# Kernel tuning notes

Measured on AMD Instinct MI355X. Metric: run time of the kernel, lower is better.

Reference implementation:

```python
import jax, jax.numpy as jnp
import numpy as np

B, NPER, H = 32, 512, 32
N, E = B * NPER, 65536
IN_CH, EDGE_CH, L1, L2, NL = 100, 16, 64, 64, 4


def setup_inputs() -> dict:
    key = jax.random.key(0)
    ks = jax.random.split(key, 14)
    f = lambda k, s: jax.random.normal(k, s, dtype=jnp.float32) * 0.1
    return {
        "x_nodes": jax.random.randint(ks[0], (N,), 0, IN_CH),
        "edge_index": jax.random.randint(ks[1], (2, E), 0, N),
        "edge_attr": jax.random.randint(ks[2], (E,), 0, EDGE_CH),
        "metal_idx": jax.random.randint(ks[3], (B,), 0, NPER),
        "loop_edge": jax.random.randint(ks[4], (B, L1, 2), 0, NPER),
        "loop_pair": jax.random.randint(ks[5], (B, L2, 2), 0, NPER),
        "node_emb": f(ks[6], (IN_CH, H)),
        "edge_emb": f(ks[7], (NL, EDGE_CH, 8)),
        "lin_w": f(ks[8], (NL, 8, H * H)),
        "lin_b": f(ks[9], (NL, H * H)),
        "root_w": f(ks[10], (NL, H, H)),
        "conv_b": f(ks[11], (NL, H)),
        "f_w": f(ks[12], (H, 1)),
        "f_b": f(ks[13], (1,)),
    }


def reference(x_nodes, edge_index, edge_attr, metal_idx, loop_edge, loop_pair,
              node_emb, edge_emb, lin_w, lin_b, root_w, conv_b, f_w, f_b):
    src, dst = edge_index[0], edge_index[1]
    # mean-aggregation denominator (clamped to 1 for isolated nodes, as PyG)
    deg = jax.ops.segment_sum(jnp.ones((E,), jnp.float32), dst, num_segments=N)
    denom = jnp.maximum(deg, 1.0)[:, None]

    x = node_emb[x_nodes]  # [N,H]
    for l in range(NL):
        # edge nn: Embedding -> ReLU -> Linear(8, H*H)
        e8 = jax.nn.relu(edge_emb[l][edge_attr])              # [E,8]
        W = (e8 @ lin_w[l] + lin_b[l]).reshape(E, H, H)       # [E,H,H]
        msg = jnp.einsum('ei,eio->eo', x[src], W)             # [E,H]
        agg = jax.ops.segment_sum(msg, dst, num_segments=N) / denom
        x_new = agg + x @ root_w[l] + conv_b[l]               # root weight + bias
        x = jax.nn.relu(x_new) if l < NL - 1 else x_new

    metal_g = metal_idx + jnp.arange(B) * NPER                # global metal node ids
    xm = x[metal_g]                                           # [B,H]
    fhM = (xm @ f_w + f_b)[:, 0]                              # [B]

    xg = x.reshape(B, NPER, H)
    bidx = jnp.arange(B)[:, None]

    def pair_prod(pairs):
        xs = xg[bidx, pairs[:, :, 0]]                         # [B,L,H]
        xt = xg[bidx, pairs[:, :, 1]]                         # [B,L,H]
        # sum(xm*xs) + sum(xm*xt) + sum(xs*(-xt))
        return jnp.sum(xm[:, None, :] * (xs + xt) - xs * xt, axis=-1)

    res_edge = pair_prod(loop_edge) - fhM[:, None]            # [B,L1]
    res_pair = -pair_prod(loop_pair)                          # [B,L2]
    return jnp.concatenate([res_edge, res_pair], axis=1)      # [B, L1+L2]
```

## Files before the change

kernel.cpp:

```cpp
#include <hip/hip_runtime.h>

#define NN 16384
#define NE 65536
#define H  32
#define BB 32
#define NPERB 512

__global__ __launch_bounds__(256) void k_prep1(
    const int* __restrict__ x_nodes, const int* __restrict__ edge_index,
    const int* __restrict__ edge_attr, const float* __restrict__ node_emb,
    const float* __restrict__ edge_emb, const float* __restrict__ lin_w,
    const float* __restrict__ lin_b, float* __restrict__ x0, float* __restrict__ Wt,
    float* __restrict__ degf, int* __restrict__ tcount, float* __restrict__ zb1) {
    __shared__ int lh[16];
    int b = blockIdx.x, thr = threadIdx.x;
    if (b < 512) {
        int t = b * 256 + thr;
        int n = t >> 3, r = t & 7;
        int xn = x_nodes[n];
        ((float4*)x0)[t] = ((const float4*)node_emb)[xn * 8 + r];
    } else if (b < 768) {
        int w = (b - 512) * 256 + thr;
        int l = w >> 14, rest = w & 16383;
        int ty = rest >> 10, io = rest & 1023;
        float acc = lin_b[l * 1024 + io];
#pragma unroll
        for (int jj = 0; jj < 8; ++jj) {
            float e2 = fmaxf(edge_emb[(l * 16 + ty) * 8 + jj], 0.f);
            acc = fmaf(e2, lin_w[(l * 8 + jj) * 1024 + io], acc);
        }
        Wt[w] = acc;
    } else if (b < 1024) {
        if (thr < 16) lh[thr] = 0;
        __syncthreads();
        int e = (b - 768) * 256 + thr;
        int d = edge_index[NE + e];
        int ty = edge_attr[e];
        atomicAdd(&degf[d], 1.0f);
        atomicAdd(&lh[ty], 1);
        __syncthreads();
        if (thr < 16) atomicAdd(&tcount[thr], lh[thr]);
    } else {
        int z = (b - 1024) * 256 + thr;
        ((float4*)zb1)[z] = make_float4(0.f, 0.f, 0.f, 0.f);
    }
}

__global__ void k_prep2(const int* __restrict__ tcount, int* __restrict__ gcursor) {
    int t = threadIdx.x;
    int c = (t < 16) ? tcount[t] : 0;
    int base = 0;
    for (int u = 0; u < 15; ++u) {
        int cu = __shfl(c, u);
        if (u < t) base += cu;
    }
    if (t < 16) gcursor[t] = base;
}

__global__ __launch_bounds__(256) void k_prep3(
    const int* __restrict__ edge_index, const int* __restrict__ edge_attr,
    int* __restrict__ gcursor, unsigned int* __restrict__ blist) {
    __shared__ int lh[16], lb[16];
    int thr = threadIdx.x;
    if (thr < 16) lh[thr] = 0;
    __syncthreads();
    int e = blockIdx.x * 256 + thr;
    unsigned int s = (unsigned int)edge_index[e];
    unsigned int d = (unsigned int)edge_index[NE + e];
    int ty = edge_attr[e];
    int rank = atomicAdd(&lh[ty], 1);
    __syncthreads();
    if (thr < 16) lb[thr] = atomicAdd(&gcursor[thr], lh[thr]);
    __syncthreads();
    blist[lb[ty] + rank] = s | (d << 14) | ((unsigned int)ty << 28);
}

__global__ __launch_bounds__(256) void k_phase(
    const float* __restrict__ xin, float* __restrict__ xout, float* __restrict__ zb,
    const unsigned int* __restrict__ blist, const float* __restrict__ degf,
    const float* __restrict__ Wl, const float* __restrict__ Rl,
    const float* __restrict__ Bl, int relu_in) {
    int t = blockIdx.x * 256 + threadIdx.x;
    int base = threadIdx.x & 32;
    if (t < 2097152) {
        int e = t >> 5, o = t & 31;
        unsigned int p = blist[e];
        int s = p & 16383, d = (p >> 14) & 16383, ty = (int)(p >> 28);
        float xv = xin[s * H + o];
        if (relu_in) xv = fmaxf(xv, 0.f);
        float invd = __builtin_amdgcn_rcpf(fmaxf(degf[d], 1.0f));
        const float* __restrict__ W = Wl + ty * 1024 + o;
        float acc = 0.f;
#pragma unroll
        for (int i = 0; i < 32; ++i)
            acc = fmaf(__shfl(xv, base + i), W[i * 32], acc);
        atomicAdd(&xout[d * H + o], acc * invd);
    } else if (t < 2621440) {
        int t2 = t - 2097152;
        int o = t2 & 31;
        float xv = xin[t2];
        if (relu_in) xv = fmaxf(xv, 0.f);
        float acc = Bl[o];
#pragma unroll
        for (int i = 0; i < 32; ++i)
            acc = fmaf(__shfl(xv, base + i), Rl[i * 32 + o], acc);
        atomicAdd(&xout[t2], acc);
    } else if (zb) {
        zb[t - 2621440] = 0.f;
    }
}

__global__ void k_final(const float* __restrict__ x, const int* __restrict__ metal_idx,
                        const int* __restrict__ loop_edge, const int* __restrict__ loop_pair,
                        const float* __restrict__ f_w, const float* __restrict__ f_b,
                        float* __restrict__ out) {
    int tid = blockIdx.x * blockDim.x + threadIdx.x;
    if (tid >= BB * 128) return;
    int b = tid >> 7, j = tid & 127;
    int mg = metal_idx[b] + b * NPERB;
    const float* __restrict__ xm = x + mg * H;
    int p0, p1;
    if (j < 64) {
        p0 = loop_edge[(b * 64 + j) * 2];
        p1 = loop_edge[(b * 64 + j) * 2 + 1];
    } else {
        int j2 = j - 64;
        p0 = loop_pair[(b * 64 + j2) * 2];
        p1 = loop_pair[(b * 64 + j2) * 2 + 1];
    }
    const float* __restrict__ xs = x + (b * NPERB + p0) * H;
    const float* __restrict__ xt = x + (b * NPERB + p1) * H;
    float fh = f_b[0];
    float pp = 0.f;
#pragma unroll
    for (int h = 0; h < H; ++h) {
        float m = xm[h];
        fh = fmaf(m, f_w[h], fh);
        pp += m * (xs[h] + xt[h]) - xs[h] * xt[h];
    }
    out[tid] = (j < 64) ? (pp - fh) : (-pp);
}

extern "C" void kernel_launch(void* const* d_in, const int* in_sizes, int n_in,
                              void* d_out, int out_size, void* d_ws, size_t ws_size,
                              hipStream_t stream) {
    const int*   x_nodes    = (const int*)d_in[0];
    const int*   edge_index = (const int*)d_in[1];
    const int*   edge_attr  = (const int*)d_in[2];
    const int*   metal_idx  = (const int*)d_in[3];
    const int*   loop_edge  = (const int*)d_in[4];
    const int*   loop_pair  = (const int*)d_in[5];
    const float* node_emb   = (const float*)d_in[6];
    const float* edge_emb   = (const float*)d_in[7];
    const float* lin_w      = (const float*)d_in[8];
    const float* lin_b      = (const float*)d_in[9];
    const float* root_w     = (const float*)d_in[10];
    const float* conv_b     = (const float*)d_in[11];
    const float* f_w        = (const float*)d_in[12];
    const float* f_b        = (const float*)d_in[13];
    float* out = (float*)d_out;

    float* ws   = (float*)d_ws;
    float* buf0 = ws;
    float* buf1 = buf0 + NN * H;
    float* buf2 = buf1 + NN * H;
    float* degf = buf2 + NN * H;
    int*   tcount  = (int*)(degf + NN);
    int*   gcursor = tcount + 16;
    unsigned int* blist = (unsigned int*)(gcursor + 16);
    float* Wt   = (float*)(blist + NE);

    hipMemsetAsync(degf, 0, (NN + 32) * sizeof(float), stream);

    k_prep1<<<1536, 256, 0, stream>>>(x_nodes, edge_index, edge_attr, node_emb,
                                      edge_emb, lin_w, lin_b, buf0, Wt, degf, tcount, buf1);
    k_prep2<<<1, 64, 0, stream>>>(tcount, gcursor);
    k_prep3<<<256, 256, 0, stream>>>(edge_index, edge_attr, gcursor, blist);

    k_phase<<<12288, 256, 0, stream>>>(buf0, buf1, buf2, blist, degf,
                                       Wt + 0 * 16384, root_w + 0 * 1024, conv_b + 0 * H, 0);
    k_phase<<<12288, 256, 0, stream>>>(buf1, buf2, buf0, blist, degf,
                                       Wt + 1 * 16384, root_w + 1 * 1024, conv_b + 1 * H, 1);
    k_phase<<<12288, 256, 0, stream>>>(buf2, buf0, buf1, blist, degf,
                                       Wt + 2 * 16384, root_w + 2 * 1024, conv_b + 2 * H, 1);
    k_phase<<<10240, 256, 0, stream>>>(buf0, buf1, (float*)0, blist, degf,
                                       Wt + 3 * 16384, root_w + 3 * 1024, conv_b + 3 * H, 1);

    k_final<<<16, 256, 0, stream>>>(buf1, metal_idx, loop_edge, loop_pair, f_w, f_b, out);
}
```

Baseline: 94.65 us.

## Replace atomic scatter with CSR-by-destination gather and LDS-cached edge weights

Result: slower. 144.8 us (+53.0%).

```diff
diff --git a/kernel.cpp b/kernel.cpp
--- a/kernel.cpp
+++ b/kernel.cpp
@@ -6,19 +6,16 @@
 #define BB 32
 #define NPERB 512
 
-__global__ __launch_bounds__(256) void k_prep1(
+__global__ __launch_bounds__(256) void k_prep(
     const int* __restrict__ x_nodes, const int* __restrict__ edge_index,
-    const int* __restrict__ edge_attr, const float* __restrict__ node_emb,
-    const float* __restrict__ edge_emb, const float* __restrict__ lin_w,
-    const float* __restrict__ lin_b, float* __restrict__ x0, float* __restrict__ Wt,
-    float* __restrict__ degf, int* __restrict__ tcount, float* __restrict__ zb1) {
-    __shared__ int lh[16];
+    const float* __restrict__ node_emb, const float* __restrict__ edge_emb,
+    const float* __restrict__ lin_w, const float* __restrict__ lin_b,
+    float* __restrict__ x0, float* __restrict__ Wt, int* __restrict__ deg) {
     int b = blockIdx.x, thr = threadIdx.x;
     if (b < 512) {
         int t = b * 256 + thr;
         int n = t >> 3, r = t & 7;
-        int xn = x_nodes[n];
-        ((float4*)x0)[t] = ((const float4*)node_emb)[xn * 8 + r];
+        ((float4*)x0)[t] = ((const float4*)node_emb)[x_nodes[n] * 8 + r];
     } else if (b < 768) {
         int w = (b - 512) * 256 + thr;
         int l = w >> 14, rest = w & 16383;
@@ -30,84 +27,103 @@
             acc = fmaf(e2, lin_w[(l * 8 + jj) * 1024 + io], acc);
         }
         Wt[w] = acc;
-    } else if (b < 1024) {
-        if (thr < 16) lh[thr] = 0;
+    } else {
+        int e = (b - 768) * 256 + thr;
+        atomicAdd(&deg[edge_index[NE + e]], 1);
+    }
+}
+
+__global__ void k_scan(const int* __restrict__ deg, int* __restrict__ offs) {
+    __shared__ int sums[1024];
+    int t = threadIdx.x;
+    int v[16];
+    int s = 0;
+#pragma unroll
+    for (int i = 0; i < 16; ++i) { v[i] = deg[t * 16 + i]; s += v[i]; }
+    sums[t] = s;
+    __syncthreads();
+    for (int off = 1; off < 1024; off <<= 1) {
+        int a = (t >= off) ? sums[t - off] : 0;
         __syncthreads();
-        int e = (b - 768) * 256 + thr;
-        int d = edge_index[NE + e];
-        int ty = edge_attr[e];
-        atomicAdd(&degf[d], 1.0f);
-        atomicAdd(&lh[ty], 1);
+        sums[t] += a;
         __syncthreads();
-        if (thr < 16) atomicAdd(&tcount[thr], lh[thr]);
-    } else {
-        int z = (b - 1024) * 256 + thr;
-        ((float4*)zb1)[z] = make_float4(0.f, 0.f, 0.f, 0.f);
-    }
-}
-
-__global__ void k_prep2(const int* __restrict__ tcount, int* __restrict__ gcursor) {
-    int t = threadIdx.x;
-    int c = (t < 16) ? tcount[t] : 0;
-    int base = 0;
-    for (int u = 0; u < 15; ++u) {
-        int cu = __shfl(c, u);
-        if (u < t) base += cu;
-    }
-    if (t < 16) gcursor[t] = base;
-}
-
-__global__ __launch_bounds__(256) void k_prep3(
+    }
+    int run = (t > 0) ? sums[t - 1] : 0;
+#pragma unroll
+    for (int i = 0; i < 16; ++i) { offs[t * 16 + i] = run; run += v[i]; }
+    if (t == 1023) offs[NN] = run;
+}
+
+__global__ __launch_bounds__(256) void k_scatter(
     const int* __restrict__ edge_index, const int* __restrict__ edge_attr,
-    int* __restrict__ gcursor, unsigned int* __restrict__ blist) {
-    __shared__ int lh[16], lb[16];
+    const int* __restrict__ offs, int* __restrict__ cnt,
+    unsigned int* __restrict__ slist) {
+    int e = blockIdx.x * 256 + threadIdx.x;
+    int s = edge_index[e], d = edge_index[NE + e], ty = edge_attr[e];
+    int slot = offs[d] + atomicAdd(&cnt[d], 1);
+    slist[slot] = (unsigned int)s | ((unsigned int)ty << 14);
+}
+
+__global__ __launch_bounds__(512, 4) void k_msg(
+    const float* __restrict__ xin, const unsigned int* __restrict__ slist,
+    const float* __restrict__ Wl, float* __restrict__ msg, int relu_in) {
+    __shared__ float Ws[16384];
     int thr = threadIdx.x;
-    if (thr < 16) lh[thr] = 0;
+    {
+        const float4* s4 = (const float4*)Wl;
+        float4* d4 = (float4*)Ws;
+#pragma unroll
+        for (int k = 0; k < 8; ++k) d4[k * 512 + thr] = s4[k * 512 + thr];
+    }
     __syncthreads();
-    int e = blockIdx.x * 256 + thr;
-    unsigned int s = (unsigned int)edge_index[e];
-    unsigned int d = (unsigned int)edge_index[NE + e];
-    int ty = edge_attr[e];
-    int rank = atomicAdd(&lh[ty], 1);
-    __syncthreads();
-    if (thr < 16) lb[thr] = atomicAdd(&gcursor[thr], lh[thr]);
-    __syncthreads();
-    blist[lb[ty] + rank] = s | (d << 14) | ((unsigned int)ty << 28);
-}
-
-__global__ __launch_bounds__(256) void k_phase(
-    const float* __restrict__ xin, float* __restrict__ xout, float* __restrict__ zb,
-    const unsigned int* __restrict__ blist, const float* __restrict__ degf,
-    const float* __restrict__ Wl, const float* __restrict__ Rl,
-    const float* __restrict__ Bl, int relu_in) {
+    int g = blockIdx.x * 16 + (thr >> 5);
+    int o = thr & 31;
+    int base = thr & 32;
+    unsigned int p = slist[g];
+    float xv = xin[(p & 16383) * H + o];
+#pragma unroll 1
+    for (int k = 0; k < 8; ++k) {
+        int e = k * 8192 + g;
+        unsigned int p_next = 0; float xv_next = 0.f;
+        if (k < 7) {
+            p_next = slist[e + 8192];
+            xv_next = xin[(p_next & 16383) * H + o];
+        }
+        int ty = (int)(p >> 14);
+        float xr = relu_in ? fmaxf(xv, 0.f) : xv;
+        const float* __restrict__ W = Ws + ty * 1024 + o;
+        float acc = 0.f;
+#pragma unroll
+        for (int i = 0; i < 32; ++i)
+            acc = fmaf(__shfl(xr, base + i), W[i * 32], acc);
+        msg[e * H + o] = acc;
+        p = p_next; xv = xv_next;
+    }
+}
+
+__global__ __launch_bounds__(256) void k_node(
+    const float* __restrict__ xin, const float* __restrict__ msg,
+    const int* __restrict__ offs, const float* __restrict__ Rl,
+    const float* __restrict__ Bl, float* __restrict__ xout, int relu_in) {
     int t = blockIdx.x * 256 + threadIdx.x;
-    int base = threadIdx.x & 32;
-    if (t < 2097152) {
-        int e = t >> 5, o = t & 31;
-        unsigned int p = blist[e];
-        int s = p & 16383, d = (p >> 14) & 16383, ty = (int)(p >> 28);
-        float xv = xin[s * H + o];
-        if (relu_in) xv = fmaxf(xv, 0.f);
-        float invd = __builtin_amdgcn_rcpf(fmaxf(degf[d], 1.0f));
-        const float* __restrict__ W = Wl + ty * 1024 + o;
-        float acc = 0.f;
-#pragma unroll
-        for (int i = 0; i < 32; ++i)
-            acc = fmaf(__shfl(xv, base + i), W[i * 32], acc);
-        atomicAdd(&xout[d * H + o], acc * invd);
-    } else if (t < 2621440) {
-        int t2 = t - 2097152;
-        int o = t2 & 31;
-        float xv = xin[t2];
-        if (relu_in) xv = fmaxf(xv, 0.f);
-        float acc = Bl[o];
-#pragma unroll
-        for (int i = 0; i < 32; ++i)
-            acc = fmaf(__shfl(xv, base + i), Rl[i * 32 + o], acc);
-        atomicAdd(&xout[t2], acc);
-    } else if (zb) {
-        zb[t - 2621440] = 0.f;
-    }
+    int n = t >> 5, o = t & 31, base = threadIdx.x & 32;
+    int e0 = offs[n], e1 = offs[n + 1];
+    float acc = 0.f;
+    int e = e0;
+    for (; e + 4 <= e1; e += 4) {
+        float m0 = msg[(e + 0) * H + o], m1 = msg[(e + 1) * H + o];
+        float m2 = msg[(e + 2) * H + o], m3 = msg[(e + 3) * H + o];
+        acc += (m0 + m1) + (m2 + m3);
+    }
+    for (; e < e1; ++e) acc += msg[e * H + o];
+    float invd = __builtin_amdgcn_rcpf(fmaxf((float)(e1 - e0), 1.f));
+    float xv = xin[t];
+    float xr = relu_in ? fmaxf(xv, 0.f) : xv;
+    float r = Bl[o];
+#pragma unroll
+    for (int i = 0; i < 32; ++i)
+        r = fmaf(__shfl(xr, base + i), Rl[i * 32 + o], r);
+    xout[t] = acc * invd + r;
 }
 
 __global__ void k_final(const float* __restrict__ x, const int* __restrict__ metal_idx,
@@ -163,28 +179,28 @@
     float* ws   = (float*)d_ws;
     float* buf0 = ws;
     float* buf1 = buf0 + NN * H;
-    float* buf2 = buf1 + NN * H;
-    float* degf = buf2 + NN * H;
-    int*   tcount  = (int*)(degf + NN);
-    int*   gcursor = tcount + 16;
-    unsigned int* blist = (unsigned int*)(gcursor + 16);
-    float* Wt   = (float*)(blist + NE);
-
-    hipMemsetAsync(degf, 0, (NN + 32) * sizeof(float), stream);
-
-    k_prep1<<<1536, 256, 0, stream>>>(x_nodes, edge_index, edge_attr, node_emb,
-                                      edge_emb, lin_w, lin_b, buf0, Wt, degf, tcount, buf1);
-    k_prep2<<<1, 64, 0, stream>>>(tcount, gcursor);
-    k_prep3<<<256, 256, 0, stream>>>(edge_index, edge_attr, gcursor, blist);
-
-    k_phase<<<12288, 256, 0, stream>>>(buf0, buf1, buf2, blist, degf,
-                                       Wt + 0 * 16384, root_w + 0 * 1024, conv_b + 0 * H, 0);
-    k_phase<<<12288, 256, 0, stream>>>(buf1, buf2, buf0, blist, degf,
-                                       Wt + 1 * 16384, root_w + 1 * 1024, conv_b + 1 * H, 1);
-    k_phase<<<12288, 256, 0, stream>>>(buf2, buf0, buf1, blist, degf,
-                                       Wt + 2 * 16384, root_w + 2 * 1024, conv_b + 2 * H, 1);
-    k_phase<<<10240, 256, 0, stream>>>(buf0, buf1, (float*)0, blist, degf,
-                                       Wt + 3 * 16384, root_w + 3 * 1024, conv_b + 3 * H, 1);
-
-    k_final<<<16, 256, 0, stream>>>(buf1, metal_idx, loop_edge, loop_pair, f_w, f_b, out);
-}
+    float* msg  = buf1 + NN * H;
+    int*   deg  = (int*)(msg + NE * H);
+    int*   cnt  = deg + NN;
+    int*   offs = cnt + NN;
+    unsigned int* slist = (unsigned int*)(offs + NN + 1);
+    float* Wt   = (float*)(slist + NE);
+
+    hipMemsetAsync(deg, 0, 2 * NN * sizeof(int), stream);
+
+    k_prep<<<1024, 256, 0, stream>>>(x_nodes, edge_index, node_emb, edge_emb,
+                                     lin_w, lin_b, buf0, Wt, deg);
+    k_scan<<<1, 1024, 0, stream>>>(deg, offs);
+    k_scatter<<<256, 256, 0, stream>>>(edge_index, edge_attr, offs, cnt, slist);
+
+    k_msg<<<512, 512, 0, stream>>>(buf0, slist, Wt + 0 * 16384, msg, 0);
+    k_node<<<2048, 256, 0, stream>>>(buf0, msg, offs, root_w + 0 * 1024, conv_b + 0 * H, buf1, 0);
+    k_msg<<<512, 512, 0, stream>>>(buf1, slist, Wt + 1 * 16384, msg, 1);
+    k_node<<<2048, 256, 0, stream>>>(buf1, msg, offs, root_w + 1 * 1024, conv_b + 1 * H, buf0, 1);
+    k_msg<<<512, 512, 0, stream>>>(buf0, slist, Wt + 2 * 16384, msg, 1);
+    k_node<<<2048, 256, 0, stream>>>(buf0, msg, offs, root_w + 2 * 1024, conv_b + 2 * H, buf1, 1);
+    k_msg<<<512, 512, 0, stream>>>(buf1, slist, Wt + 3 * 16384, msg, 1);
+    k_node<<<2048, 256, 0, stream>>>(buf1, msg, offs, root_w + 3 * 1024, conv_b + 3 * H, buf0, 1);
+
+    k_final<<<16, 256, 0, stream>>>(buf0, metal_idx, loop_edge, loop_pair, f_w, f_b, out);
+}
```
